# Kernel tuning notes

Hardware: AMD Instinct MI355X
Metric: run time of the kernel (lower is better)

Reference implementation:

```python
import jax, jax.numpy as jnp
import numpy as np

NEG_SLOPE = 0.2  # PyG GATConv default negative_slope


def gat_layer(x, src, dst, N, W, att_src, att_dst, bias, heads, out_ch, concat):
    # x: [N, Fin]; W: [Fin, heads*out_ch]; att_*: [heads, out_ch]; bias matches output dim
    h = (x @ W).reshape(N, heads, out_ch)              # [N, H, C]
    a_src = (h * att_src).sum(-1)                      # [N, H]
    a_dst = (h * att_dst).sum(-1)                      # [N, H]
    e = jax.nn.leaky_relu(a_src[src] + a_dst[dst], NEG_SLOPE)  # [E, H]
    # segment softmax over incoming edges of each destination node
    e_max = jax.ops.segment_max(e, dst, num_segments=N)        # [N, H]
    e_exp = jnp.exp(e - e_max[dst])                             # [E, H]
    denom = jax.ops.segment_sum(e_exp, dst, num_segments=N)    # [N, H]
    alpha = e_exp / (denom[dst] + 1e-16)                        # [E, H]
    msg = alpha[:, :, None] * h[src]                            # [E, H, C]
    out = jax.ops.segment_sum(msg, dst, num_segments=N)        # [N, H, C]
    out = out.reshape(N, heads * out_ch) if concat else out.mean(axis=1)
    return out + bias


def setup_inputs() -> dict:
    key = jax.random.key(0)
    ks = jax.random.split(key, 10)
    N, E = 40000, 160000
    Fin, H1, C1 = 602, 8, 256
    H2, C2 = 1, 42
    g = lambda k, shape, fan: (jax.random.normal(k, shape, dtype=jnp.float32) * (1.0 / np.sqrt(fan)))
    return {
        "x": jax.random.normal(ks[0], (N, Fin), dtype=jnp.float32),
        "edge_index": jax.random.randint(ks[1], (2, E), 0, N, dtype=jnp.int64),
        "W1": g(ks[2], (Fin, H1 * C1), Fin),
        "att_src1": g(ks[3], (H1, C1), C1),
        "att_dst1": g(ks[4], (H1, C1), C1),
        "b1": jnp.zeros((H1 * C1,), dtype=jnp.float32),
        "W2": g(ks[5], (H1 * C1, H2 * C2), H1 * C1),
        "att_src2": g(ks[6], (H2, C2), C2),
        "att_dst2": g(ks[7], (H2, C2), C2),
        "b2": jnp.zeros((C2,), dtype=jnp.float32),
    }


def reference(x, edge_index, W1, att_src1, att_dst1, b1, W2, att_src2, att_dst2, b2):
    N = x.shape[0]
    # PyG GATConv default add_self_loops=True
    loops = jnp.arange(N, dtype=edge_index.dtype)
    src = jnp.concatenate([edge_index[0], loops])
    dst = jnp.concatenate([edge_index[1], loops])
    h = gat_layer(x, src, dst, N, W1, att_src1, att_dst1, b1, heads=8, out_ch=256, concat=True)
    h = jax.nn.relu(h)  # dropout is identity in eval mode
    h = gat_layer(h, src, dst, N, W2, att_src2, att_dst2, b2, heads=1, out_ch=42, concat=False)
    return jax.nn.log_softmax(h, axis=1)
```

## Files before the change

### kernel.cpp

```cpp
#include <hip/hip_runtime.h>
#include <hip/hip_bf16.h>

#define NN   40000
#define NE   160000
#define ETOT 200000
#define FIN  602
#define NH1  8
#define C1   256
#define F1   2048
#define C2   42
#define NEG  0.2f
#define NB   157
#define KP   608
#define MP   40064

typedef unsigned short u16;
typedef unsigned int   u32;
typedef __bf16 bf16x8 __attribute__((ext_vector_type(8)));
typedef float  f32x4  __attribute__((ext_vector_type(4)));

__device__ __forceinline__ float bfu(u16 v){ return __uint_as_float(((u32)v) << 16); }
__device__ __forceinline__ float bflo(u32 u){ return __uint_as_float(u << 16); }
__device__ __forceinline__ float bfhi(u32 u){ return __uint_as_float(u & 0xffff0000u); }
__device__ __forceinline__ u16 f2bf(float f){
  u32 u = __float_as_uint(f);
  u32 r = (u + 0x7fffu + ((u >> 16) & 1u)) >> 16;
  return (u16)r;
}

__device__ __forceinline__ void gl_lds16(const u16* g, u16* l) {
  __builtin_amdgcn_global_load_lds(
      (const __attribute__((address_space(1))) u32*)(g),
      (__attribute__((address_space(3))) u32*)(l), 16, 0, 0);
}

__global__ void probe_k(const u32* __restrict__ xw, const int* __restrict__ ei,
                        int* __restrict__ flags) {
  if (threadIdx.x == 0) {
    int zc = 0;
    for (int k = 0; k < 64; ++k) zc += (ei[2*k + 1] == 0) ? 1 : 0;
    flags[0] = (zc == 64) ? 1 : 0;
    int inr = 0;
    for (int k = 0; k < 64; ++k) {
      u32 low = xw[k] & 0xffffu;
      int e = (int)((low >> 7) & 0xff);
      inr += (e >= 100 && e <= 140) ? 1 : 0;
    }
    flags[1] = (inr >= 32) ? 0 : 1;
  }
}

__global__ void cvt_f32_k(const void* __restrict__ src, float* __restrict__ dst, int n,
                          const int* __restrict__ flags) {
  int i = blockIdx.x * 256 + threadIdx.x;
  if (i >= n) return;
  dst[i] = flags[1] ? ((const float*)src)[i] : bfu(((const u16*)src)[i]);
}

__global__ void xb_k(const void* __restrict__ x, u16* __restrict__ xb,
                     const int* __restrict__ flags) {
  int k = blockIdx.x * 256 + threadIdx.x;
  int row = blockIdx.y;
  if (k >= KP) return;
  u16 v = 0;
  if (row < NN && k < FIN)
    v = flags[1] ? f2bf(((const float*)x)[(size_t)row * FIN + k])
                 : ((const u16*)x)[(size_t)row * FIN + k];
  xb[(size_t)row * KP + k] = v;
}

__global__ void w1t_k(const void* __restrict__ W1, u16* __restrict__ w1t,
                      const int* __restrict__ flags) {
  int n = blockIdx.x * 256 + threadIdx.x;
  int k = blockIdx.y;
  if (n >= F1) return;
  u16 v = 0;
  if (k < FIN) v = flags[1] ? f2bf(((const float*)W1)[(size_t)k * F1 + n])
                            : ((const u16*)W1)[(size_t)k * F1 + n];
  w1t[(size_t)n * KP + k] = v;
}

__global__ void w2t_k(const void* __restrict__ W2, u16* __restrict__ w2t,
                      const int* __restrict__ flags) {
  int i = blockIdx.x * 256 + threadIdx.x;
  if (i >= 64 * F1) return;
  int c = i >> 11, k = i & (F1 - 1);
  u16 v = 0;
  if (c < C2) v = flags[1] ? f2bf(((const float*)W2)[(size_t)k * C2 + c])
                           : ((const u16*)W2)[(size_t)k * C2 + c];
  w2t[i] = v;
}

__device__ __forceinline__ void edge_sd(const int* __restrict__ ei, int e, int imode,
                                        int& s, int& d) {
  if (e < NE) {
    if (imode) { s = ei[2*e]; d = ei[2*(NE + e)]; }
    else       { s = ei[e];   d = ei[NE + e];     }
  } else { s = d = e - NE; }
}

__global__ void deg_k(const int* __restrict__ ei, int* __restrict__ deg,
                      const int* __restrict__ flags) {
  int e = blockIdx.x * 256 + threadIdx.x;
  if (e >= ETOT) return;
  int s, d; edge_sd(ei, e, flags[0], s, d);
  atomicAdd(&deg[d], 1);
}

__global__ __launch_bounds__(256) void scan1_k(const int* __restrict__ deg,
                                               int* __restrict__ tmp, int* __restrict__ bsum) {
  __shared__ int s[256];
  int b = blockIdx.x, t = threadIdx.x, i = b * 256 + t;
  int v = (i < NN) ? deg[i] : 0;
  s[t] = v; __syncthreads();
  for (int o = 1; o < 256; o <<= 1) {
    int u = (t >= o) ? s[t - o] : 0;
    __syncthreads(); s[t] += u; __syncthreads();
  }
  if (i < NN) tmp[i] = s[t];
  if (t == 255) bsum[b] = s[255];
}

__global__ __launch_bounds__(256) void scan2_k(int* __restrict__ bsum) {
  __shared__ int s[256];
  int t = threadIdx.x;
  int v = (t < NB) ? bsum[t] : 0;
  s[t] = v; __syncthreads();
  for (int o = 1; o < 256; o <<= 1) {
    int u = (t >= o) ? s[t - o] : 0;
    __syncthreads(); s[t] += u; __syncthreads();
  }
  if (t < NB) bsum[t] = s[t];
}

__global__ void scan3_k(const int* __restrict__ deg, const int* __restrict__ tmp,
                        const int* __restrict__ bsum, int* __restrict__ start, int* __restrict__ cur) {
  int i = blockIdx.x * 256 + threadIdx.x;
  if (i >= NN) return;
  int b = i >> 8;
  int off = b ? bsum[b - 1] : 0;
  int excl = tmp[i] - deg[i] + off;
  start[i] = excl; cur[i] = excl;
}

__global__ void fill_k(const int* __restrict__ ei, int* __restrict__ cur,
                       int* __restrict__ csr_src, int* __restrict__ csr_dst,
                       const int* __restrict__ flags) {
  int e = blockIdx.x * 256 + threadIdx.x;
  if (e >= ETOT) return;
  int s, d; edge_sd(ei, e, flags[0], s, d);
  int pos = atomicAdd(&cur[d], 1);
  csr_src[pos] = s; csr_dst[pos] = d;
}

__global__ __launch_bounds__(256) void gemm1a_k(const u16* __restrict__ xb,
                                                const u16* __restrict__ w1t,
                                                u16* __restrict__ h1,
                                                const float* __restrict__ as1c,
                                                const float* __restrict__ ad1c,
                                                float* __restrict__ a_s1,
                                                float* __restrict__ a_d1) {
  __shared__ u16 As[2 * 4096];
  __shared__ u16 Bs[2 * 4096];
  const int t = threadIdx.x;
  const int lane = t & 63, wid = t >> 6;
  const int wr = wid >> 1, wc = wid & 1;
  const int m0 = blockIdx.y * 128, n0 = blockIdx.x * 128;
  const int l16 = lane & 15;
  f32x4 acc[4][4];
  #pragma unroll
  for (int i = 0; i < 4; ++i)
    #pragma unroll
    for (int j = 0; j < 4; ++j) acc[i][j] = (f32x4){0.f, 0.f, 0.f, 0.f};

  const int kc = (((t & 3) ^ ((t >> 3) & 3))) * 8;
  const size_t sa0 = (size_t)(m0 + (t >> 2)) * KP + kc;
  const size_t sa1 = (size_t)(m0 + 64 + (t >> 2)) * KP + kc;
  const size_t sb0 = (size_t)(n0 + (t >> 2)) * KP + kc;
  const size_t sb1 = (size_t)(n0 + 64 + (t >> 2)) * KP + kc;

  const int fsw = ((lane >> 4) ^ ((l16 >> 1) & 3)) << 3;
  const int rdA = (wr * 64 + l16) * 32 + fsw;
  const int rdB = (wc * 64 + l16) * 32 + fsw;

#define STAGE(K0, B) do {                                      \
    u16* a_ = As + (B) * 4096 + (wid << 9);                    \
    u16* b_ = Bs + (B) * 4096 + (wid << 9);                    \
    gl_lds16(xb  + sa0 + (K0), a_);                            \
    gl_lds16(xb  + sa1 + (K0), a_ + 2048);                     \
    gl_lds16(w1t + sb0 + (K0), b_);                            \
    gl_lds16(w1t + sb1 + (K0), b_ + 2048);                     \
  } while (0)

  STAGE(0, 0);
  __syncthreads();
  int cur = 0;
  for (int k0 = 0; k0 < KP; k0 += 32) {
    if (k0 + 32 < KP) STAGE(k0 + 32, cur ^ 1);
    const u16* Ab = As + cur * 4096;
    const u16* Bb = Bs + cur * 4096;
    bf16x8 bfr[4];
    #pragma unroll
    for (int ni = 0; ni < 4; ++ni)
      bfr[ni] = *(const bf16x8*)&Bb[rdB + ni * 512];
    #pragma unroll
    for (int mi = 0; mi < 4; ++mi) {
      bf16x8 af = *(const bf16x8*)&Ab[rdA + mi * 512];
      #pragma unroll
      for (int ni = 0; ni < 4; ++ni)
        acc[mi][ni] = __builtin_amdgcn_mfma_f32_16x16x32_bf16(af, bfr[ni], acc[mi][ni], 0, 0, 0);
    }
    __syncthreads();
    cur ^= 1;
  }
#undef STAGE

  const int h0 = n0 >> 8;
  float psrc[4][4], pdst[4][4];
  #pragma unroll
  for (int mi = 0; mi < 4; ++mi)
    #pragma unroll
    for (int r = 0; r < 4; ++r) { psrc[mi][r] = 0.f; pdst[mi][r] = 0.f; }
  #pragma unroll
  for (int ni = 0; ni < 4; ++ni) {
    int col = n0 + wc * 64 + ni * 16 + l16;
    float wsv = as1c[col], wdv = ad1c[col];
    #pragma unroll
    for (int mi = 0; mi < 4; ++mi)
      #pragma unroll
      for (int r = 0; r < 4; ++r) {
        float v = acc[mi][ni][r];
        psrc[mi][r] += v * wsv;
        pdst[mi][r] += v * wdv;
      }
  }
  #pragma unroll
  for (int o = 1; o < 16; o <<= 1) {
    #pragma unroll
    for (int mi = 0; mi < 4; ++mi)
      #pragma unroll
      for (int r = 0; r < 4; ++r) {
        psrc[mi][r] += __shfl_xor(psrc[mi][r], o, 64);
        pdst[mi][r] += __shfl_xor(pdst[mi][r], o, 64);
      }
  }
  const int lr4 = (lane >> 4) * 4;
  if (l16 == 0) {
    #pragma unroll
    for (int mi = 0; mi < 4; ++mi)
      #pragma unroll
      for (int r = 0; r < 4; ++r) {
        int row = m0 + wr * 64 + mi * 16 + lr4 + r;
        if (row < NN) {
          atomicAdd(&a_s1[row * NH1 + h0], psrc[mi][r]);
          atomicAdd(&a_d1[row * NH1 + h0], pdst[mi][r]);
        }
      }
  }

  #pragma unroll
  for (int mi = 0; mi < 4; ++mi) {
    #pragma unroll
    for (int r = 0; r < 4; ++r) {
      int row = m0 + wr * 64 + mi * 16 + lr4 + r;
      if (row < NN) {
        #pragma unroll
        for (int ni = 0; ni < 4; ++ni) {
          int col = n0 + wc * 64 + ni * 16 + l16;
          h1[(size_t)row * F1 + col] = f2bf(acc[mi][ni][r]);
        }
      }
    }
  }
}

__global__ __launch_bounds__(256) void gemm1m_k(const void* __restrict__ xv,
                                                const u16* __restrict__ w1t,
                                                u16* __restrict__ h1,
                                                const int* __restrict__ flags) {
  __shared__ u16 As[128][40];
  __shared__ u16 Bs[128][40];
  const int fm = flags[1];
  const int t = threadIdx.x;
  const int lane = t & 63, wid = t >> 6;
  const int wr = wid >> 1, wc = wid & 1;
  const int m0 = blockIdx.y * 128, n0 = blockIdx.x * 128;
  const int l16 = lane & 15, lk = (lane >> 4) * 8;
  f32x4 acc[4][4];
  #pragma unroll
  for (int i = 0; i < 4; ++i)
    #pragma unroll
    for (int j = 0; j < 4; ++j) acc[i][j] = (f32x4){0.f, 0.f, 0.f, 0.f};
  const int arow = t >> 2;
  const int akb  = (t & 3) * 8;
  for (int k0 = 0; k0 < KP; k0 += 32) {
    #pragma unroll
    for (int i = 0; i < 2; ++i) {
      int row = arow + i * 64;
      int rg = m0 + row;
      u32 d0 = 0, d1 = 0, d2 = 0, d3 = 0;
      if (rg < NN) {
        if (k0 + 32 <= FIN) {
          if (fm) {
            const float* xp = (const float*)xv + (size_t)rg * FIN + k0 + akb;
            float2 p0 = *(const float2*)(xp);
            float2 p1 = *(const float2*)(xp + 2);
            float2 p2 = *(const float2*)(xp + 4);
            float2 p3 = *(const float2*)(xp + 6);
            d0 = (u32)f2bf(p0.x) | ((u32)f2bf(p0.y) << 16);
            d1 = (u32)f2bf(p1.x) | ((u32)f2bf(p1.y) << 16);
            d2 = (u32)f2bf(p2.x) | ((u32)f2bf(p2.y) << 16);
            d3 = (u32)f2bf(p3.x) | ((u32)f2bf(p3.y) << 16);
          } else {
            const u16* xp = (const u16*)xv + (size_t)rg * FIN + k0 + akb;
            d0 = *(const u32*)(xp);
            d1 = *(const u32*)(xp + 2);
            d2 = *(const u32*)(xp + 4);
            d3 = *(const u32*)(xp + 6);
          }
        } else {
          u16 e[8];
          #pragma unroll
          for (int q = 0; q < 8; ++q) {
            int k = k0 + akb + q;
            e[q] = 0;
            if (k < FIN)
              e[q] = fm ? f2bf(((const float*)xv)[(size_t)rg * FIN + k])
                        : ((const u16*)xv)[(size_t)rg * FIN + k];
          }
          d0 = (u32)e[0] | ((u32)e[1] << 16);
          d1 = (u32)e[2] | ((u32)e[3] << 16);
          d2 = (u32)e[4] | ((u32)e[5] << 16);
          d3 = (u32)e[6] | ((u32)e[7] << 16);
        }
      }
      *(uint4*)&As[row][akb] = make_uint4(d0, d1, d2, d3);
      const u16* wp = w1t + (size_t)(n0 + row) * KP + k0 + akb;
      *(uint4*)&Bs[row][akb] = *(const uint4*)wp;
    }
    __syncthreads();
    bf16x8 bfr[4];
    #pragma unroll
    for (int ni = 0; ni < 4; ++ni)
      bfr[ni] = *(const bf16x8*)&Bs[wc * 64 + ni * 16 + l16][lk];
    #pragma unroll
    for (int mi = 0; mi < 4; ++mi) {
      bf16x8 af = *(const bf16x8*)&As[wr * 64 + mi * 16 + l16][lk];
      #pragma unroll
      for (int ni = 0; ni < 4; ++ni)
        acc[mi][ni] = __builtin_amdgcn_mfma_f32_16x16x32_bf16(af, bfr[ni], acc[mi][ni], 0, 0, 0);
    }
    __syncthreads();
  }
  const int lr4 = (lane >> 4) * 4;
  #pragma unroll
  for (int mi = 0; mi < 4; ++mi) {
    #pragma unroll
    for (int r = 0; r < 4; ++r) {
      int row = m0 + wr * 64 + mi * 16 + lr4 + r;
      if (row < NN) {
        #pragma unroll
        for (int ni = 0; ni < 4; ++ni) {
          int col = n0 + wc * 64 + ni * 16 + l16;
          h1[(size_t)row * F1 + col] = f2bf(acc[mi][ni][r]);
        }
      }
    }
  }
}

__global__ __launch_bounds__(256) void att1_k(const u16* __restrict__ h1,
                                              const float* __restrict__ as1c, const float* __restrict__ ad1c,
                                              float* __restrict__ a_s, float* __restrict__ a_d) {
  int n = blockIdx.x, t = threadIdx.x;
  int h = t >> 5, l = t & 31;
  int base = h * C1 + l * 8;
  const u16* hp = h1 + (size_t)n * F1 + base;
  uint4 v = *(const uint4*)hp;
  u32 w[4] = {v.x, v.y, v.z, v.w};
  float ss = 0.f, sd = 0.f;
  #pragma unroll
  for (int p = 0; p < 4; ++p) {
    float e0 = bflo(w[p]), e1 = bfhi(w[p]);
    ss += e0 * as1c[base + 2*p] + e1 * as1c[base + 2*p + 1];
    sd += e0 * ad1c[base + 2*p] + e1 * ad1c[base + 2*p + 1];
  }
  #pragma unroll
  for (int o = 16; o > 0; o >>= 1) {
    ss += __shfl_down(ss, o, 32);
    sd += __shfl_down(sd, o, 32);
  }
  if (l == 0) { a_s[n * NH1 + h] = ss; a_d[n * NH1 + h] = sd; }
}

__global__ __launch_bounds__(256) void gfuse_k(const int* __restrict__ start, const int* __restrict__ deg,
                                               const int* __restrict__ csr_src,
                                               const float* __restrict__ a_s1, const float* __restrict__ a_d1,
                                               const u16* __restrict__ h1, const float* __restrict__ b1c,
                                               const u16* __restrict__ w2t, float* __restrict__ h2) {
  __shared__ u16 rowsL[16 * F1];
  int t = threadIdx.x;
  int nb = blockIdx.x * 16;
  int h = t >> 5;
  int c0 = t * 8;
  float4 bA = *(const float4*)(b1c + c0);
  float4 bB = *(const float4*)(b1c + c0 + 4);
  for (int i = 0; i < 16; ++i) {
    int n = nb + i;
    int s0 = start[n], jend = s0 + deg[n];
    float ad = a_d1[n * NH1 + h];
    float a0=0.f,a1=0.f,a2=0.f,a3=0.f,a4=0.f,a5=0.f,a6=0.f,a7=0.f,den=0.f;
    int j = s0;
    for (; j + 2 <= jend; j += 2) {
      int sA = csr_src[j], sB = csr_src[j + 1];
      float vA = a_s1[sA * NH1 + h] + ad;
      float vB = a_s1[sB * NH1 + h] + ad;
      vA = vA > 0.f ? vA : NEG * vA;
      vB = vB > 0.f ? vB : NEG * vB;
      float eA = expf(vA), eB = expf(vB);
      uint4 uA = *(const uint4*)(h1 + (size_t)sA * F1 + c0);
      uint4 uB = *(const uint4*)(h1 + (size_t)sB * F1 + c0);
      den += eA + eB;
      a0 += eA * bflo(uA.x) + eB * bflo(uB.x);
      a1 += eA * bfhi(uA.x) + eB * bfhi(uB.x);
      a2 += eA * bflo(uA.y) + eB * bflo(uB.y);
      a3 += eA * bfhi(uA.y) + eB * bfhi(uB.y);
      a4 += eA * bflo(uA.z) + eB * bflo(uB.z);
      a5 += eA * bfhi(uA.z) + eB * bfhi(uB.z);
      a6 += eA * bflo(uA.w) + eB * bflo(uB.w);
      a7 += eA * bfhi(uA.w) + eB * bfhi(uB.w);
    }
    if (j < jend) {
      int sA = csr_src[j];
      float vA = a_s1[sA * NH1 + h] + ad;
      vA = vA > 0.f ? vA : NEG * vA;
      float eA = expf(vA);
      uint4 uA = *(const uint4*)(h1 + (size_t)sA * F1 + c0);
      den += eA;
      a0 += eA * bflo(uA.x); a1 += eA * bfhi(uA.x);
      a2 += eA * bflo(uA.y); a3 += eA * bfhi(uA.y);
      a4 += eA * bflo(uA.z); a5 += eA * bfhi(uA.z);
      a6 += eA * bflo(uA.w); a7 += eA * bfhi(uA.w);
    }
    float inv = 1.f / (den + 1e-16f);
    u16 o0 = f2bf(fmaxf(a0 * inv + bA.x, 0.f));
    u16 o1 = f2bf(fmaxf(a1 * inv + bA.y, 0.f));
    u16 o2 = f2bf(fmaxf(a2 * inv + bA.z, 0.f));
    u16 o3 = f2bf(fmaxf(a3 * inv + bA.w, 0.f));
    u16 o4 = f2bf(fmaxf(a4 * inv + bB.x, 0.f));
    u16 o5 = f2bf(fmaxf(a5 * inv + bB.y, 0.f));
    u16 o6 = f2bf(fmaxf(a6 * inv + bB.z, 0.f));
    u16 o7 = f2bf(fmaxf(a7 * inv + bB.w, 0.f));
    uint4 pk;
    pk.x = (u32)o0 | ((u32)o1 << 16);
    pk.y = (u32)o2 | ((u32)o3 << 16);
    pk.z = (u32)o4 | ((u32)o5 << 16);
    pk.w = (u32)o6 | ((u32)o7 << 16);
    int sw = (i & 7) << 3;
    *(uint4*)&rowsL[i * F1 + (c0 ^ sw)] = pk;
  }
  __syncthreads();
  int lane = t & 63, wid = t >> 6;
  int l16 = lane & 15, lk = (lane >> 4) * 8;
  const u16* wt = w2t + (size_t)(wid * 16 + l16) * F1;
  int sw = (l16 & 7) << 3;
  f32x4 acc2 = (f32x4){0.f, 0.f, 0.f, 0.f};
  for (int k0 = 0; k0 < F1; k0 += 32) {
    int kk = k0 + lk;
    bf16x8 af = *(const bf16x8*)&rowsL[l16 * F1 + (kk ^ sw)];
    bf16x8 bf = *(const bf16x8*)(wt + kk);
    acc2 = __builtin_amdgcn_mfma_f32_16x16x32_bf16(af, bf, acc2, 0, 0, 0);
  }
  int col = wid * 16 + l16;
  if (col < C2) {
    int mb = (lane >> 4) * 4;
    #pragma unroll
    for (int r = 0; r < 4; ++r)
      h2[(size_t)(nb + mb + r) * C2 + col] = acc2[r];
  }
}

__global__ __launch_bounds__(64) void att2_k(const float* __restrict__ h2,
                                             const float* __restrict__ as2, const float* __restrict__ ad2,
                                             float* __restrict__ a_s, float* __restrict__ a_d) {
  int n = blockIdx.x, t = threadIdx.x;
  float ss = 0.f, sd = 0.f;
  if (t < C2) {
    float v = h2[(size_t)n * C2 + t];
    ss = v * as2[t];
    sd = v * ad2[t];
  }
  #pragma unroll
  for (int o = 32; o > 0; o >>= 1) {
    ss += __shfl_down(ss, o, 64);
    sd += __shfl_down(sd, o, 64);
  }
  if (t == 0) { a_s[n] = ss; a_d[n] = sd; }
}

__global__ __launch_bounds__(64) void gath2_k(const int* __restrict__ start, const int* __restrict__ deg,
                                              const int* __restrict__ csr_src,
                                              const float* __restrict__ a_s, const float* __restrict__ a_d,
                                              const float* __restrict__ h2, const float* __restrict__ b2,
                                              void* __restrict__ outv, const int* __restrict__ flags) {
  int n = blockIdx.x, t = threadIdx.x;
  int s0 = start[n], cnt = deg[n];
  float ad = a_d[n];
  float acc = 0.f, den = 0.f;
  for (int j = s0; j < s0 + cnt; ++j) {
    int s = csr_src[j];
    float v = a_s[s] + ad;
    v = v > 0.f ? v : NEG * v;
    float e = expf(v);
    den += e;
    if (t < C2) acc += e * h2[(size_t)s * C2 + t];
  }
  float raw = (t < C2) ? acc / (den + 1e-16f) + b2[t] : -1e30f;
  float m = raw;
  #pragma unroll
  for (int o = 32; o > 0; o >>= 1) m = fmaxf(m, __shfl_down(m, o, 64));
  m = __shfl(m, 0, 64);
  float e2 = (t < C2) ? expf(raw - m) : 0.f;
  float ssum = e2;
  #pragma unroll
  for (int o = 32; o > 0; o >>= 1) ssum += __shfl_down(ssum, o, 64);
  ssum = __shfl(ssum, 0, 64);
  if (t < C2) {
    float v = raw - m - logf(ssum);
    if (flags[1]) ((float*)outv)[(size_t)n * C2 + t] = v;
    else          ((u16*) outv)[(size_t)n * C2 + t] = f2bf(v);
  }
}

extern "C" void kernel_launch(void* const* d_in, const int* in_sizes, int n_in,
                              void* d_out, int out_size, void* d_ws, size_t ws_size,
                              hipStream_t stream) {
  const void* x   = d_in[0];
  const int*  ei  = (const int*)d_in[1];
  const void* W1  = d_in[2];
  const void* as1 = d_in[3];
  const void* ad1 = d_in[4];
  const void* b1  = d_in[5];
  const void* W2  = d_in[6];
  const void* as2 = d_in[7];
  const void* ad2 = d_in[8];
  const void* b2  = d_in[9];

  char* ws = (char*)d_ws;
  u16*   h1      = (u16*)  (ws);
  float* ex1     = (float*)(ws + 163840000);
  float* h2      = (float*)(ws + 170240000);
  float* a_s1    = (float*)(ws + 176960000);
  float* a_d1    = (float*)(ws + 178240000);
  float* a_s2    = (float*)(ws + 179520000);
  float* a_d2    = (float*)(ws + 179680000);
  int*   deg     = (int*)  (ws + 179840000);
  int*   start   = (int*)  (ws + 180000000);
  int*   cur     = (int*)  (ws + 180160000);
  int*   tmp     = (int*)  (ws + 180320000);
  int*   csr_src = (int*)  (ws + 180480000);
  int*   csr_dst = (int*)  (ws + 181280000);
  int*   bsum    = (int*)  (ws + 182080000);
  u16*   w1t     = (u16*)  (ws + 182081024);
  u16*   w2t     = (u16*)  (ws + 184571392);
  float* as1c    = (float*)(ws + 184833536);
  float* ad1c    = (float*)(ws + 184841728);
  float* b1c     = (float*)(ws + 184849920);
  float* as2c    = (float*)(ws + 184858112);
  float* ad2c    = (float*)(ws + 184858368);
  float* b2c     = (float*)(ws + 184858624);
  int*   flags   = (int*)  (ws + 184858880);
  const size_t TOTAL_BASE = 184859136;
  u16*   xb      = (u16*)  (ws + TOTAL_BASE);
  const size_t TOTAL_A = TOTAL_BASE + (size_t)MP * KP * 2;
  if (ws_size < TOTAL_BASE) return;
  const bool pathA = (ws_size >= TOTAL_A);
  (void)ex1;

  probe_k<<<1, 64, 0, stream>>>((const u32*)x, ei, flags);

  cvt_f32_k<<<(F1 + 255) / 256, 256, 0, stream>>>(as1, as1c, F1, flags);
  cvt_f32_k<<<(F1 + 255) / 256, 256, 0, stream>>>(ad1, ad1c, F1, flags);
  cvt_f32_k<<<(F1 + 255) / 256, 256, 0, stream>>>(b1, b1c, F1, flags);
  cvt_f32_k<<<1, 256, 0, stream>>>(as2, as2c, C2, flags);
  cvt_f32_k<<<1, 256, 0, stream>>>(ad2, ad2c, C2, flags);
  cvt_f32_k<<<1, 256, 0, stream>>>(b2, b2c, C2, flags);
  w1t_k<<<dim3(8, KP), 256, 0, stream>>>(W1, w1t, flags);
  w2t_k<<<(64 * F1 + 255) / 256, 256, 0, stream>>>(W2, w2t, flags);

  hipMemsetAsync(deg, 0, NN * sizeof(int), stream);
  hipMemsetAsync(a_s1, 0, 2 * NN * NH1 * sizeof(float), stream);
  const int EB = (ETOT + 255) / 256;
  deg_k  <<<EB, 256, 0, stream>>>(ei, deg, flags);
  scan1_k<<<NB, 256, 0, stream>>>(deg, tmp, bsum);
  scan2_k<<<1, 256, 0, stream>>>(bsum);
  scan3_k<<<NB, 256, 0, stream>>>(deg, tmp, bsum, start, cur);
  fill_k <<<EB, 256, 0, stream>>>(ei, cur, csr_src, csr_dst, flags);

  if (pathA) {
    xb_k<<<dim3((KP + 255) / 256, MP), 256, 0, stream>>>(x, xb, flags);
    gemm1a_k<<<dim3(16, MP / 128), 256, 0, stream>>>(xb, w1t, h1, as1c, ad1c, a_s1, a_d1);
  } else {
    gemm1m_k<<<dim3(16, MP / 128), 256, 0, stream>>>(x, w1t, h1, flags);
    att1_k<<<NN, 256, 0, stream>>>(h1, as1c, ad1c, a_s1, a_d1);
  }
  gfuse_k<<<NN / 16, 256, 0, stream>>>(start, deg, csr_src, a_s1, a_d1, h1, b1c, w2t, h2);

  att2_k<<<NN, 64, 0, stream>>>(h2, as2c, ad2c, a_s2, a_d2);
  gath2_k<<<NN, 64, 0, stream>>>(start, deg, csr_src, a_s2, a_d2, h2, b2c, d_out, flags);
}
```

Measured before the change: 688.0 us.

## Enlarge GEMM1 tile to 256x256 with 512 threads and split gfuse K

```diff
diff --git a/kernel.cpp b/kernel.cpp
--- a/kernel.cpp
+++ b/kernel.cpp
@@ -12,7 +12,7 @@
 #define NEG  0.2f
 #define NB   157
 #define KP   608
-#define MP   40064
+#define MP   40192
 
 typedef unsigned short u16;
 typedef unsigned int   u32;
@@ -153,43 +153,43 @@
   csr_src[pos] = s; csr_dst[pos] = d;
 }
 
-__global__ __launch_bounds__(256) void gemm1a_k(const u16* __restrict__ xb,
+__global__ __launch_bounds__(512) void gemm1c_k(const u16* __restrict__ xb,
                                                 const u16* __restrict__ w1t,
                                                 u16* __restrict__ h1,
                                                 const float* __restrict__ as1c,
                                                 const float* __restrict__ ad1c,
                                                 float* __restrict__ a_s1,
                                                 float* __restrict__ a_d1) {
-  __shared__ u16 As[2 * 4096];
-  __shared__ u16 Bs[2 * 4096];
+  __shared__ u16 As[2 * 8192];
+  __shared__ u16 Bs[2 * 8192];
   const int t = threadIdx.x;
   const int lane = t & 63, wid = t >> 6;
-  const int wr = wid >> 1, wc = wid & 1;
-  const int m0 = blockIdx.y * 128, n0 = blockIdx.x * 128;
+  const int wr = wid >> 2, wc = wid & 3;
+  const int m0 = blockIdx.y * 256, n0 = blockIdx.x * 256;
   const int l16 = lane & 15;
-  f32x4 acc[4][4];
-  #pragma unroll
-  for (int i = 0; i < 4; ++i)
+  f32x4 acc[8][4];
+  #pragma unroll
+  for (int i = 0; i < 8; ++i)
     #pragma unroll
     for (int j = 0; j < 4; ++j) acc[i][j] = (f32x4){0.f, 0.f, 0.f, 0.f};
 
-  const int kc = (((t & 3) ^ ((t >> 3) & 3))) * 8;
+  const int kc = ((t & 3) ^ ((t >> 3) & 3)) * 8;
   const size_t sa0 = (size_t)(m0 + (t >> 2)) * KP + kc;
-  const size_t sa1 = (size_t)(m0 + 64 + (t >> 2)) * KP + kc;
+  const size_t sa1 = sa0 + (size_t)128 * KP;
   const size_t sb0 = (size_t)(n0 + (t >> 2)) * KP + kc;
-  const size_t sb1 = (size_t)(n0 + 64 + (t >> 2)) * KP + kc;
+  const size_t sb1 = sb0 + (size_t)128 * KP;
 
   const int fsw = ((lane >> 4) ^ ((l16 >> 1) & 3)) << 3;
-  const int rdA = (wr * 64 + l16) * 32 + fsw;
+  const int rdA = (wr * 128 + l16) * 32 + fsw;
   const int rdB = (wc * 64 + l16) * 32 + fsw;
 
-#define STAGE(K0, B) do {                                      \
-    u16* a_ = As + (B) * 4096 + (wid << 9);                    \
-    u16* b_ = Bs + (B) * 4096 + (wid << 9);                    \
-    gl_lds16(xb  + sa0 + (K0), a_);                            \
-    gl_lds16(xb  + sa1 + (K0), a_ + 2048);                     \
-    gl_lds16(w1t + sb0 + (K0), b_);                            \
-    gl_lds16(w1t + sb1 + (K0), b_ + 2048);                     \
+#define STAGE(K0, B) do {                                  \
+    u16* a_ = As + (B) * 8192 + (wid << 9);                \
+    u16* b_ = Bs + (B) * 8192 + (wid << 9);                \
+    gl_lds16(xb  + sa0 + (K0), a_);                        \
+    gl_lds16(xb  + sa1 + (K0), a_ + 4096);                 \
+    gl_lds16(w1t + sb0 + (K0), b_);                        \
+    gl_lds16(w1t + sb1 + (K0), b_ + 4096);                 \
   } while (0)
 
   STAGE(0, 0);
@@ -197,14 +197,14 @@
   int cur = 0;
   for (int k0 = 0; k0 < KP; k0 += 32) {
     if (k0 + 32 < KP) STAGE(k0 + 32, cur ^ 1);
-    const u16* Ab = As + cur * 4096;
-    const u16* Bb = Bs + cur * 4096;
+    const u16* Ab = As + cur * 8192;
+    const u16* Bb = Bs + cur * 8192;
     bf16x8 bfr[4];
     #pragma unroll
     for (int ni = 0; ni < 4; ++ni)
       bfr[ni] = *(const bf16x8*)&Bb[rdB + ni * 512];
     #pragma unroll
-    for (int mi = 0; mi < 4; ++mi) {
+    for (int mi = 0; mi < 8; ++mi) {
       bf16x8 af = *(const bf16x8*)&Ab[rdA + mi * 512];
       #pragma unroll
       for (int ni = 0; ni < 4; ++ni)
@@ -216,53 +216,43 @@
 #undef STAGE
 
   const int h0 = n0 >> 8;
-  float psrc[4][4], pdst[4][4];
-  #pragma unroll
-  for (int mi = 0; mi < 4; ++mi)
-    #pragma unroll
-    for (int r = 0; r < 4; ++r) { psrc[mi][r] = 0.f; pdst[mi][r] = 0.f; }
-  #pragma unroll
-  for (int ni = 0; ni < 4; ++ni) {
-    int col = n0 + wc * 64 + ni * 16 + l16;
-    float wsv = as1c[col], wdv = ad1c[col];
-    #pragma unroll
-    for (int mi = 0; mi < 4; ++mi)
+  const int lr4 = (lane >> 4) * 4;
+  #pragma unroll
+  for (int mi = 0; mi < 8; ++mi) {
+    float ps[4] = {0.f, 0.f, 0.f, 0.f}, pd[4] = {0.f, 0.f, 0.f, 0.f};
+    #pragma unroll
+    for (int ni = 0; ni < 4; ++ni) {
+      int col = n0 + wc * 64 + ni * 16 + l16;
+      float wsv = as1c[col], wdv = ad1c[col];
       #pragma unroll
       for (int r = 0; r < 4; ++r) {
         float v = acc[mi][ni][r];
-        psrc[mi][r] += v * wsv;
-        pdst[mi][r] += v * wdv;
+        ps[r] += v * wsv;
+        pd[r] += v * wdv;
       }
-  }
-  #pragma unroll
-  for (int o = 1; o < 16; o <<= 1) {
-    #pragma unroll
-    for (int mi = 0; mi < 4; ++mi)
+    }
+    #pragma unroll
+    for (int o = 1; o < 16; o <<= 1) {
       #pragma unroll
       for (int r = 0; r < 4; ++r) {
-        psrc[mi][r] += __shfl_xor(psrc[mi][r], o, 64);
-        pdst[mi][r] += __shfl_xor(pdst[mi][r], o, 64);
+        ps[r] += __shfl_xor(ps[r], o, 64);
+        pd[r] += __shfl_xor(pd[r], o, 64);
       }
-  }
-  const int lr4 = (lane >> 4) * 4;
-  if (l16 == 0) {
-    #pragma unroll
-    for (int mi = 0; mi < 4; ++mi)
+    }
+    int rowb = m0 + wr * 128 + mi * 16 + lr4;
+    if (l16 == 0) {
       #pragma unroll
       for (int r = 0; r < 4; ++r) {
-        int row = m0 + wr * 64 + mi * 16 + lr4 + r;
+        int row = rowb + r;
         if (row < NN) {
-          atomicAdd(&a_s1[row * NH1 + h0], psrc[mi][r]);
-          atomicAdd(&a_d1[row * NH1 + h0], pdst[mi][r]);
+          atomicAdd(&a_s1[row * NH1 + h0], ps[r]);
+          atomicAdd(&a_d1[row * NH1 + h0], pd[r]);
         }
       }
-  }
-
-  #pragma unroll
-  for (int mi = 0; mi < 4; ++mi) {
+    }
     #pragma unroll
     for (int r = 0; r < 4; ++r) {
-      int row = m0 + wr * 64 + mi * 16 + lr4 + r;
+      int row = rowb + r;
       if (row < NN) {
         #pragma unroll
         for (int ni = 0; ni < 4; ++ni) {
@@ -393,19 +383,22 @@
   if (l == 0) { a_s[n * NH1 + h] = ss; a_d[n * NH1 + h] = sd; }
 }
 
-__global__ __launch_bounds__(256) void gfuse_k(const int* __restrict__ start, const int* __restrict__ deg,
+__global__ __launch_bounds__(512) void gfuse_k(const int* __restrict__ start, const int* __restrict__ deg,
                                                const int* __restrict__ csr_src,
                                                const float* __restrict__ a_s1, const float* __restrict__ a_d1,
                                                const u16* __restrict__ h1, const float* __restrict__ b1c,
                                                const u16* __restrict__ w2t, float* __restrict__ h2) {
   __shared__ u16 rowsL[16 * F1];
+  __shared__ float pb[4][16][16];
   int t = threadIdx.x;
   int nb = blockIdx.x * 16;
-  int h = t >> 5;
-  int c0 = t * 8;
+  int sub = t & 255, grp = t >> 8;
+  int h = sub >> 5;
+  int c0 = sub * 8;
   float4 bA = *(const float4*)(b1c + c0);
   float4 bB = *(const float4*)(b1c + c0 + 4);
-  for (int i = 0; i < 16; ++i) {
+  for (int ii = 0; ii < 8; ++ii) {
+    int i = grp * 8 + ii;
     int n = nb + i;
     int s0 = start[n], jend = s0 + deg[n];
     float ad = a_d1[n * NH1 + h];
@@ -461,22 +454,31 @@
   }
   __syncthreads();
   int lane = t & 63, wid = t >> 6;
+  int g = wid & 3, kh = wid >> 2;
   int l16 = lane & 15, lk = (lane >> 4) * 8;
-  const u16* wt = w2t + (size_t)(wid * 16 + l16) * F1;
+  const u16* wt = w2t + (size_t)(g * 16 + l16) * F1;
   int sw = (l16 & 7) << 3;
   f32x4 acc2 = (f32x4){0.f, 0.f, 0.f, 0.f};
-  for (int k0 = 0; k0 < F1; k0 += 32) {
-    int kk = k0 + lk;
+  const int kbase = kh * (F1 / 2);
+  for (int k0 = 0; k0 < F1 / 2; k0 += 32) {
+    int kk = kbase + k0 + lk;
     bf16x8 af = *(const bf16x8*)&rowsL[l16 * F1 + (kk ^ sw)];
     bf16x8 bf = *(const bf16x8*)(wt + kk);
     acc2 = __builtin_amdgcn_mfma_f32_16x16x32_bf16(af, bf, acc2, 0, 0, 0);
   }
-  int col = wid * 16 + l16;
-  if (col < C2) {
-    int mb = (lane >> 4) * 4;
-    #pragma unroll
-    for (int r = 0; r < 4; ++r)
-      h2[(size_t)(nb + mb + r) * C2 + col] = acc2[r];
+  int mb = (lane >> 4) * 4;
+  if (kh == 1) {
+    #pragma unroll
+    for (int r = 0; r < 4; ++r) pb[g][mb + r][l16] = acc2[r];
+  }
+  __syncthreads();
+  if (kh == 0) {
+    int col = g * 16 + l16;
+    if (col < C2) {
+      #pragma unroll
+      for (int r = 0; r < 4; ++r)
+        h2[(size_t)(nb + mb + r) * C2 + col] = acc2[r] + pb[g][mb + r][l16];
+    }
   }
 }
 
@@ -548,34 +550,32 @@
 
   char* ws = (char*)d_ws;
   u16*   h1      = (u16*)  (ws);
-  float* ex1     = (float*)(ws + 163840000);
-  float* h2      = (float*)(ws + 170240000);
-  float* a_s1    = (float*)(ws + 176960000);
-  float* a_d1    = (float*)(ws + 178240000);
-  float* a_s2    = (float*)(ws + 179520000);
-  float* a_d2    = (float*)(ws + 179680000);
-  int*   deg     = (int*)  (ws + 179840000);
-  int*   start   = (int*)  (ws + 180000000);
-  int*   cur     = (int*)  (ws + 180160000);
-  int*   tmp     = (int*)  (ws + 180320000);
-  int*   csr_src = (int*)  (ws + 180480000);
-  int*   csr_dst = (int*)  (ws + 181280000);
-  int*   bsum    = (int*)  (ws + 182080000);
-  u16*   w1t     = (u16*)  (ws + 182081024);
-  u16*   w2t     = (u16*)  (ws + 184571392);
-  float* as1c    = (float*)(ws + 184833536);
-  float* ad1c    = (float*)(ws + 184841728);
-  float* b1c     = (float*)(ws + 184849920);
-  float* as2c    = (float*)(ws + 184858112);
-  float* ad2c    = (float*)(ws + 184858368);
-  float* b2c     = (float*)(ws + 184858624);
-  int*   flags   = (int*)  (ws + 184858880);
-  const size_t TOTAL_BASE = 184859136;
+  float* h2      = (float*)(ws + 163840000);
+  float* a_s1    = (float*)(ws + 170560000);
+  float* a_d1    = (float*)(ws + 171840000);
+  float* a_s2    = (float*)(ws + 173120000);
+  float* a_d2    = (float*)(ws + 173280000);
+  int*   deg     = (int*)  (ws + 173440000);
+  int*   start   = (int*)  (ws + 173600000);
+  int*   cur     = (int*)  (ws + 173760000);
+  int*   tmp     = (int*)  (ws + 173920000);
+  int*   csr_src = (int*)  (ws + 174080000);
+  int*   csr_dst = (int*)  (ws + 174880000);
+  int*   bsum    = (int*)  (ws + 175680000);
+  u16*   w1t     = (u16*)  (ws + 175681024);
+  u16*   w2t     = (u16*)  (ws + 178171392);
+  float* as1c    = (float*)(ws + 178433536);
+  float* ad1c    = (float*)(ws + 178441728);
+  float* b1c     = (float*)(ws + 178449920);
+  float* as2c    = (float*)(ws + 178458112);
+  float* ad2c    = (float*)(ws + 178458368);
+  float* b2c     = (float*)(ws + 178458624);
+  int*   flags   = (int*)  (ws + 178458880);
+  const size_t TOTAL_BASE = 178459136;
   u16*   xb      = (u16*)  (ws + TOTAL_BASE);
   const size_t TOTAL_A = TOTAL_BASE + (size_t)MP * KP * 2;
   if (ws_size < TOTAL_BASE) return;
   const bool pathA = (ws_size >= TOTAL_A);
-  (void)ex1;
 
   probe_k<<<1, 64, 0, stream>>>((const u32*)x, ei, flags);
 
@@ -599,12 +599,12 @@
 
   if (pathA) {
     xb_k<<<dim3((KP + 255) / 256, MP), 256, 0, stream>>>(x, xb, flags);
-    gemm1a_k<<<dim3(16, MP / 128), 256, 0, stream>>>(xb, w1t, h1, as1c, ad1c, a_s1, a_d1);
+    gemm1c_k<<<dim3(8, MP / 256), 512, 0, stream>>>(xb, w1t, h1, as1c, ad1c, a_s1, a_d1);
   } else {
-    gemm1m_k<<<dim3(16, MP / 128), 256, 0, stream>>>(x, w1t, h1, flags);
+    gemm1m_k<<<dim3(16, 313), 256, 0, stream>>>(x, w1t, h1, flags);
     att1_k<<<NN, 256, 0, stream>>>(h1, as1c, ad1c, a_s1, a_d1);
   }
-  gfuse_k<<<NN / 16, 256, 0, stream>>>(start, deg, csr_src, a_s1, a_d1, h1, b1c, w2t, h2);
+  gfuse_k<<<NN / 16, 512, 0, stream>>>(start, deg, csr_src, a_s1, a_d1, h1, b1c, w2t, h2);
 
   att2_k<<<NN, 64, 0, stream>>>(h2, as2c, ad2c, a_s2, a_d2);
   gath2_k<<<NN, 64, 0, stream>>>(start, deg, csr_src, a_s2, a_d2, h2, b2c, d_out, flags);
```

New measurement: 641.7 us. 6.7% less time.
